# Kernel tuning notes

Hardware: AMD Instinct MI355X
Metric: run time of the kernel (lower is better)

## Reference

```python
import jax, jax.numpy as jnp
import numpy as np

INV_SQRT2 = 0.7071067811865476
BETA = 0.3
LN_EPS = 1e-5

B, S, P, C, TD = 128, 1024, 336, 128, 4
H1, H2, K = C // 4, C // 8, 3  # rda=4, rdb=8, ksize=3


def setup_inputs() -> dict:
    key = jax.random.key(0)
    ks = jax.random.split(key, 20)
    rn = lambda k, sh: jax.random.normal(k, sh, dtype=jnp.float32)
    return {
        "x": rn(ks[0], (B, S, C)),
        "x_mark_enc": rn(ks[1], (B, S, TD)),
        "x_dec": rn(ks[2], (B, P, C)),
        "y_mark_dec": rn(ks[3], (B, P, TD)),
        # time_enc params
        "W1": rn(ks[4], (H1, TD)) * 0.1, "b1": jnp.zeros((H1,), jnp.float32),
        "g1": jnp.ones((H1,), jnp.float32), "be1": jnp.zeros((H1,), jnp.float32),
        "W2": rn(ks[5], (H2, H1)) * 0.1, "b2": jnp.zeros((H2,), jnp.float32),
        "g2": jnp.ones((H2,), jnp.float32), "be2": jnp.zeros((H2,), jnp.float32),
        "Wc": rn(ks[6], (S, S, K)) * 0.02, "bc": jnp.zeros((S,), jnp.float32),
        "W3": rn(ks[7], (C, H2)) * 0.1, "b3": jnp.zeros((C,), jnp.float32),
        # projections
        "Wtp": rn(ks[8], (P, S)) * 0.02, "btp": jnp.zeros((P,), jnp.float32),
        "Whp": rn(ks[9], (P, S)) * 0.02, "bhp": jnp.zeros((P,), jnp.float32),
    }


def _haar_level1(x):
    # pywt.wavedec(sig, 'db1', level=1) -> [cA, cD]; concat along time.
    # For even length: cA[k]=(x[2k]+x[2k+1])/sqrt(2), cD[k]=(x[2k]-x[2k+1])/sqrt(2).
    xe, xo = x[:, 0::2, :], x[:, 1::2, :]
    cA = (xe + xo) * INV_SQRT2
    cD = (xe - xo) * INV_SQRT2
    return jnp.concatenate([cA, cD], axis=1)  # [B, S, C]


def _layernorm(h, g, b):
    m = jnp.mean(h, axis=-1, keepdims=True)
    v = jnp.mean((h - m) ** 2, axis=-1, keepdims=True)
    return (h - m) * jax.lax.rsqrt(v + LN_EPS) * g + b


def reference(x, x_mark_enc, x_dec, y_mark_dec,
              W1, b1, g1, be1, W2, b2, g2, be2, Wc, bc, W3, b3,
              Wtp, btp, Whp, bhp):
    # wavelet transform + instance norm over time (torch.var is unbiased)
    xw = _haar_level1(x)
    means = jnp.mean(xw, axis=1, keepdims=True)
    stdev = jnp.sqrt(jnp.var(xw, axis=1, ddof=1, keepdims=True) + 1e-5)
    xn = (xw - means) / stdev

    # time_enc MLP: Linear -> LN -> ReLU -> Linear -> LN -> ReLU
    h = jax.nn.relu(_layernorm(jnp.einsum('bst,ht->bsh', x_mark_enc, W1) + b1, g1, be1))
    h = jax.nn.relu(_layernorm(jnp.einsum('bsh,gh->bsg', h, W2) + b2, g2, be2))
    # Conv1d(in=seq_len, out=seq_len, k=3, padding='same') over feature dim H2
    h = jax.lax.conv_general_dilated(h, Wc, window_strides=(1,), padding='SAME',
                                     dimension_numbers=('NCH', 'OIH', 'NCH'))
    h = h + bc[None, :, None]
    time_embed = jnp.einsum('bsg,cg->bsc', h, W3) + b3  # [B, S, C]

    # seq->pred projections (Linear over time axis), then blend
    time_out = jnp.einsum('bsc,ps->bpc', time_embed, Wtp) + btp[None, :, None]
    pred = jnp.einsum('bsc,ps->bpc', xn, Whp) + bhp[None, :, None]
    pred = BETA * pred + (1.0 - BETA) * time_out
    pred = pred * stdev + means
    return pred  # [B, P, C] == dec_out[:, -pred_len:, :]
```

## Files before the change

kernel.cpp:

```cpp
#include <hip/hip_runtime.h>
#include <hip/hip_bf16.h>

#define INV_SQRT2f 0.70710678118654752440f
#define BETAf 0.3f
#define OMBf  0.7f
#define LN_EPSf 1e-5f

#define B 128
#define S 1024
#define P 336
#define C 128
#define H1 32
#define H2 16

#define WS_WHP2G  0
#define WS_EPI    262144
#define WS_BCP    296448
#define WS_H2     296832
#define WS_WCPT   2393984
#define WS_M      2393984
#define WS_AIMG   3426176

typedef short  s16x8 __attribute__((ext_vector_type(8)));
typedef float  f32x4 __attribute__((ext_vector_type(4)));

__device__ __forceinline__ unsigned f2bf(float f) {
    unsigned u = __float_as_uint(f);
    return (u + 0x7fffu + ((u >> 16) & 1u)) >> 16;
}

__device__ __forceinline__ int whp2l_u32(int p, int sp) {
    int kt   = sp >> 4;
    int tile = kt * 2 + p / 192;
    int sub  = (p % 192) >> 4;
    int kg   = (sp & 15) >> 2;
    int m    = p & 15;
    int byte = tile * 12288 + sub * 1024 + kg * 256 + m * 16 + 4 * (sp & 3);
    return byte >> 2;
}

__global__ void k_prep(const float* __restrict__ Whp, const float* __restrict__ Wtp,
                       const float* __restrict__ bc,  const float* __restrict__ bhp,
                       const float* __restrict__ btp, float* __restrict__ ws)
{
    const int p = blockIdx.x;
    const int t = threadIdx.x;
    unsigned* img = (unsigned*)ws;
    __shared__ float red[768];
    float sw = 0.f, rw = 0.f, bp = 0.f;
    for (int sp = t; sp < 512; sp += 256) {
        float a = Whp[p * 1024 + sp];
        float d = Whp[p * 1024 + 512 + sp];
        float va = BETAf * (a + d) * INV_SQRT2f;
        float vb = BETAf * (a - d) * INV_SQRT2f;
        img[whp2l_u32(p, sp)] = f2bf(va) | (f2bf(vb) << 16);
        sw += a + d;
    }
    for (int s = t; s < S; s += 256) {
        float w = Wtp[p * 1024 + s];
        rw += w;
        bp += w * bc[s];
    }
    red[t] = sw; red[256 + t] = rw; red[512 + t] = bp;
    __syncthreads();
    for (int off = 128; off > 0; off >>= 1) {
        if (t < off) {
            red[t]       += red[t + off];
            red[256 + t] += red[256 + t + off];
            red[512 + t] += red[512 + t + off];
        }
        __syncthreads();
    }
    if (t == 0) {
        ws[WS_BCP + p] = red[512];
        float* e = ws + WS_EPI + p * 4;
        e[0] = BETAf * bhp[p] + OMBf * btp[p];
        e[1] = OMBf * red[256];
        e[2] = 1.f - BETAf * red[0];
        e[3] = 0.f;
    }
}

__global__ void k_mlp(const float* __restrict__ xme,
                      const float* __restrict__ W1, const float* __restrict__ b1,
                      const float* __restrict__ g1, const float* __restrict__ be1,
                      const float* __restrict__ W2, const float* __restrict__ b2,
                      const float* __restrict__ g2, const float* __restrict__ be2,
                      float* __restrict__ ws)
{
    __shared__ float w1s[128], b1s[32], g1s[32], be1s[32];
    __shared__ float w2s[512], b2s[16], g2s[16], be2s[16];
    const int t = threadIdx.x;
    if (t < 128) w1s[t] = W1[t];
    if (t < 32) { b1s[t] = b1[t]; g1s[t] = g1[t]; be1s[t] = be1[t]; }
    for (int i = t; i < 512; i += 256) w2s[i] = W2[i];
    if (t < 16) { b2s[t] = b2[t]; g2s[t] = g2[t]; be2s[t] = be2[t]; }
    __syncthreads();

    const int row = blockIdx.x * 256 + t;
    float4 v = *(const float4*)(xme + (size_t)row * 4);

    float h1v[32];
    float m = 0.f;
    #pragma unroll
    for (int i = 0; i < 32; i++) {
        float a = w1s[i*4+0]*v.x + w1s[i*4+1]*v.y + w1s[i*4+2]*v.z + w1s[i*4+3]*v.w + b1s[i];
        h1v[i] = a; m += a;
    }
    m *= (1.f / 32.f);
    float var = 0.f;
    #pragma unroll
    for (int i = 0; i < 32; i++) { float d = h1v[i] - m; var += d * d; }
    var *= (1.f / 32.f);
    float rs = rsqrtf(var + LN_EPSf);
    #pragma unroll
    for (int i = 0; i < 32; i++)
        h1v[i] = fmaxf((h1v[i] - m) * rs * g1s[i] + be1s[i], 0.f);

    float h2v[16];
    float m2 = 0.f;
    #pragma unroll
    for (int g = 0; g < 16; g++) {
        float a = b2s[g];
        #pragma unroll
        for (int i = 0; i < 32; i++) a = fmaf(w2s[g * 32 + i], h1v[i], a);
        h2v[g] = a; m2 += a;
    }
    m2 *= (1.f / 16.f);
    float v2 = 0.f;
    #pragma unroll
    for (int g = 0; g < 16; g++) { float d = h2v[g] - m2; v2 += d * d; }
    v2 *= (1.f / 16.f);
    float rs2 = rsqrtf(v2 + LN_EPSf);
    float* h2o = ws + WS_H2 + (size_t)row * 16;
    #pragma unroll
    for (int g = 0; g < 16; g++)
        h2o[g] = fmaxf((h2v[g] - m2) * rs2 * g2s[g] + be2s[g], 0.f);
}

__global__ __launch_bounds__(256) void k_wcp(const float* __restrict__ Wc,
                                             const float* __restrict__ Wtp,
                                             float* __restrict__ ws)
{
    __shared__ __align__(16) unsigned short Bs[2][4][4][16][8];
    const int pbase = blockIdx.x * 96;
    const int n0    = blockIdx.y * 64;
    const int t     = threadIdx.x;
    const int lane  = t & 63;
    const int wid   = t >> 6;
    const int wm    = wid >> 1;
    const int wn    = wid & 1;
    const int g8    = lane >> 4;
    const int n16   = lane & 15;

    const int bn  = t & 63;
    const int bkg = t >> 6;

    int prow[3];
    #pragma unroll
    for (int fi = 0; fi < 3; fi++) {
        int pr = pbase + wm * 48 + fi * 16 + n16;
        prow[fi] = pr < P ? pr : P - 1;
    }

#define LOADB_(dst, kt) {                                                   \
    const float* xs_ = Wc + (size_t)((kt) * 32 + 8 * bkg) * 3072 + n0 + bn; \
    _Pragma("unroll")                                                       \
    for (int e_ = 0; e_ < 8; e_++) dst[e_] = xs_[(size_t)e_ * 3072]; }

#define WRITEB_(src, buf) {                                                 \
    uint4 w_;                                                               \
    w_.x = f2bf(src[0]) | (f2bf(src[1]) << 16);                             \
    w_.y = f2bf(src[2]) | (f2bf(src[3]) << 16);                             \
    w_.z = f2bf(src[4]) | (f2bf(src[5]) << 16);                             \
    w_.w = f2bf(src[6]) | (f2bf(src[7]) << 16);                             \
    *(uint4*)&Bs[buf][bn >> 4][bkg][bn & 15][0] = w_; }

#define LOADA_(dst, kt) {                                                   \
    _Pragma("unroll")                                                       \
    for (int fi_ = 0; fi_ < 3; fi_++) {                                     \
        const float* as_ = Wtp + (size_t)prow[fi_] * 1024 + (kt) * 32 + g8 * 8; \
        dst[fi_][0] = *(const float4*)(as_);                                \
        dst[fi_][1] = *(const float4*)(as_ + 4); } }

#define PACKA_(fa, src) {                                                   \
    _Pragma("unroll")                                                       \
    for (int fi_ = 0; fi_ < 3; fi_++) {                                     \
        uint4 w_;                                                           \
        w_.x = f2bf(src[fi_][0].x) | (f2bf(src[fi_][0].y) << 16);           \
        w_.y = f2bf(src[fi_][0].z) | (f2bf(src[fi_][0].w) << 16);           \
        w_.z = f2bf(src[fi_][1].x) | (f2bf(src[fi_][1].y) << 16);           \
        w_.w = f2bf(src[fi_][1].z) | (f2bf(src[fi_][1].w) << 16);           \
        fa[fi_] = *(s16x8*)&w_; } }

#define MFMA6_(buf, fa) {                                                   \
    s16x8 fb0 = *(const s16x8*)&Bs[buf][2 * wn + 0][g8][n16][0];            \
    s16x8 fb1 = *(const s16x8*)&Bs[buf][2 * wn + 1][g8][n16][0];            \
    _Pragma("unroll")                                                       \
    for (int fi_ = 0; fi_ < 3; fi_++) {                                     \
        acc[fi_][0] = __builtin_amdgcn_mfma_f32_16x16x32_bf16(fa[fi_], fb0, acc[fi_][0], 0, 0, 0); \
        acc[fi_][1] = __builtin_amdgcn_mfma_f32_16x16x32_bf16(fa[fi_], fb1, acc[fi_][1], 0, 0, 0); } }

    f32x4 acc[3][2];
    #pragma unroll
    for (int i = 0; i < 3; i++) {
        acc[i][0] = (f32x4){0.f, 0.f, 0.f, 0.f};
        acc[i][1] = (f32x4){0.f, 0.f, 0.f, 0.f};
    }

    float  b0r[8], b1r[8];
    float4 a0r[3][2], a1r[3][2];

    LOADA_(a0r, 0); LOADB_(b0r, 0);
    LOADA_(a1r, 1); LOADB_(b1r, 1);
    WRITEB_(b0r, 0);
    __syncthreads();

    for (int i = 0; i < 16; i++) {
        const int kt = 2 * i;
        {
            s16x8 fa[3];
            PACKA_(fa, a0r);
            if (kt + 2 < 32) { LOADA_(a0r, kt + 2); LOADB_(b0r, kt + 2); }
            MFMA6_(0, fa);
        }
        __syncthreads();
        WRITEB_(b1r, 1);
        __syncthreads();
        {
            s16x8 fa[3];
            PACKA_(fa, a1r);
            if (kt + 3 < 32) { LOADA_(a1r, kt + 3); LOADB_(b1r, kt + 3); }
            MFMA6_(1, fa);
        }
        __syncthreads();
        if (kt + 2 < 32) WRITEB_(b0r, 0);
        __syncthreads();
    }

#undef LOADB_
#undef WRITEB_
#undef LOADA_
#undef PACKA_
#undef MFMA6_

    float* wcT = ws + WS_WCPT;
    #pragma unroll
    for (int fi = 0; fi < 3; fi++) {
        #pragma unroll
        for (int r = 0; r < 4; r++) {
            int p = pbase + wm * 48 + fi * 16 + g8 * 4 + r;
            if (p < P) {
                wcT[(size_t)p * 3072 + n0 + wn * 32 + 0 * 16 + n16] = acc[fi][0][r];
                wcT[(size_t)p * 3072 + n0 + wn * 32 + 1 * 16 + n16] = acc[fi][1][r];
            }
        }
    }
}

__global__ void k_repack(float* __restrict__ ws)
{
    const int l  = threadIdx.x;
    const int ch = blockIdx.x;
    const int pf = blockIdx.y;
    const int k  = ch >> 5;
    const int i0 = (ch & 31) * 32 + (l >> 4) * 8;
    const int p  = pf * 16 + (l & 15);
    uint4 w = make_uint4(0, 0, 0, 0);
    if (p < P) {
        const float* wcT = ws + WS_WCPT + (size_t)p * 3072;
        float v[8];
        #pragma unroll
        for (int e = 0; e < 8; e++)
            v[e] = wcT[(i0 + e) * 3 + k];
        w.x = f2bf(v[0]) | (f2bf(v[1]) << 16);
        w.y = f2bf(v[2]) | (f2bf(v[3]) << 16);
        w.z = f2bf(v[4]) | (f2bf(v[5]) << 16);
        w.w = f2bf(v[6]) | (f2bf(v[7]) << 16);
    }
    ((uint4*)(ws + WS_AIMG))[(size_t)(ch * 24 + pf) * 64 + l] = w;
}

#define HT_RS 1056
__global__ __launch_bounds__(256) void k_mconv(float* __restrict__ ws)
{
    __shared__ unsigned short Ht[18 * HT_RS];
    const int b  = blockIdx.x;
    const int pt = blockIdx.y;
    const int t  = threadIdx.x;
    const int l  = t & 63;
    const int wid = t >> 6;
    const int pf = pt * 4 + wid;
    const int n16 = l & 15;
    const int g8  = l >> 4;

    for (int j = t; j < HT_RS; j += 256) {
        Ht[j] = 0;
        Ht[17 * HT_RS + j] = 0;
    }
    {
        const float* h2b = ws + WS_H2 + (size_t)b * 16384;
        const int s0 = t * 4;
        float v[4][16];
        #pragma unroll
        for (int rr = 0; rr < 4; rr++) {
            const float4* src = (const float4*)(h2b + (size_t)(s0 + rr) * 16);
            float4 a0 = src[0], a1 = src[1], a2 = src[2], a3 = src[3];
            v[rr][0]=a0.x; v[rr][1]=a0.y; v[rr][2]=a0.z; v[rr][3]=a0.w;
            v[rr][4]=a1.x; v[rr][5]=a1.y; v[rr][6]=a1.z; v[rr][7]=a1.w;
            v[rr][8]=a2.x; v[rr][9]=a2.y; v[rr][10]=a2.z; v[rr][11]=a2.w;
            v[rr][12]=a3.x; v[rr][13]=a3.y; v[rr][14]=a3.z; v[rr][15]=a3.w;
        }
        #pragma unroll
        for (int g = 0; g < 16; g++) {
            uint2 w;
            w.x = f2bf(v[0][g]) | (f2bf(v[1][g]) << 16);
            w.y = f2bf(v[2][g]) | (f2bf(v[3][g]) << 16);
            *(uint2*)&Ht[(g + 1) * HT_RS + s0] = w;
        }
    }
    __syncthreads();

    const uint4* ap = (const uint4*)(ws + WS_AIMG) + (size_t)pf * 64 + l;
    f32x4 acc = (f32x4){0.f, 0.f, 0.f, 0.f};
    uint4 fan = *ap;
    #pragma unroll 4
    for (int it = 0; it < 96; it++) {
        uint4 fac = fan;
        ap += 24 * 64;
        if (it < 95) fan = *ap;
        const int k  = it >> 5;
        const int kt = it & 31;
        s16x8 fb = *(const s16x8*)&Ht[(n16 + k) * HT_RS + kt * 32 + g8 * 8];
        s16x8 fa = *(s16x8*)&fac;
        acc = __builtin_amdgcn_mfma_f32_16x16x32_bf16(fa, fb, acc, 0, 0, 0);
    }

    #pragma unroll
    for (int r = 0; r < 4; r++) {
        int p = pf * 16 + g8 * 4 + r;
        if (p < P)
            ws[WS_M + ((size_t)b * P + p) * 16 + n16] = acc[r] + ws[WS_BCP + p];
    }
}

__global__ __launch_bounds__(256, 2) void k_pred(
    const float* __restrict__ x,
    const float* __restrict__ W3, const float* __restrict__ b3,
    const float* __restrict__ ws, float* __restrict__ out)
{
    __shared__ __align__(16) unsigned short Bs[2][8][4][16][8];
    __shared__ float sev[256], ssq[256], smean[128], sstd[128];
    const int b     = blockIdx.x;
    const int ptile = blockIdx.y;
    const int t     = threadIdx.x;
    const int lane  = t & 63;
    const int wid   = t >> 6;
    const int wm    = wid >> 1;
    const int wn    = wid & 1;
    const int g8    = lane >> 4;
    const int n16   = lane & 15;

    const float* xb = x + (size_t)b * S * C;
    const char* aimgc = (const char*)ws
        + ((ptile >> 1) * 12288)
        + (((ptile & 1) * 6 + wm * 3) * 1024)
        + (g8 * 256 + n16 * 16);

    f32x4 acc[3][4];
    #pragma unroll
    for (int i = 0; i < 3; i++)
        #pragma unroll
        for (int j = 0; j < 4; j++) acc[i][j] = (f32x4){0.f, 0.f, 0.f, 0.f};

    float ev_acc = 0.f, sq_acc = 0.f;

#define P_LOADB_(dst, kt) {                                                 \
    _Pragma("unroll")                                                       \
    for (int i_ = 0; i_ < 2; i_++) {                                        \
        int chunk_ = i_ * 256 + t;                                          \
        int c_ = chunk_ & 127, kg_ = chunk_ >> 7;                           \
        const float* xs_ = xb + (size_t)(32 * (kt) + 8 * kg_) * C + c_;     \
        _Pragma("unroll")                                                   \
        for (int e_ = 0; e_ < 8; e_++) dst[i_][e_] = xs_[(size_t)e_ * C]; } }

#define P_WRITEB_(src, buf) {                                               \
    _Pragma("unroll")                                                       \
    for (int i_ = 0; i_ < 2; i_++) {                                        \
        int chunk_ = i_ * 256 + t;                                          \
        int c_ = chunk_ & 127, kg_ = chunk_ >> 7;                           \
        uint4 w_;                                                           \
        w_.x = f2bf(src[i_][0]) | (f2bf(src[i_][1]) << 16);                 \
        w_.y = f2bf(src[i_][2]) | (f2bf(src[i_][3]) << 16);                 \
        w_.z = f2bf(src[i_][4]) | (f2bf(src[i_][5]) << 16);                 \
        w_.w = f2bf(src[i_][6]) | (f2bf(src[i_][7]) << 16);                 \
        *(uint4*)&Bs[buf][c_ >> 4][kg_][c_ & 15][0] = w_;                   \
        _Pragma("unroll")                                                   \
        for (int e_ = 0; e_ < 8; e_++) {                                    \
            float v_ = src[i_][e_];                                         \
            sq_acc = fmaf(v_, v_, sq_acc);                                  \
            if ((e_ & 1) == 0) ev_acc += v_;    \
        } } }

#define P_LOADA_(dst, kt) {                                                 \
    const char* ap_ = aimgc + (size_t)(kt) * 24576;                         \
    _Pragma("unroll")                                                       \
    for (int fi_ = 0; fi_ < 3; fi_++)                                       \
        dst[fi_] = *(const uint4*)(ap_ + fi_ * 1024); }

#define P_MFMA_(buf, au) {                                                  \
    s16x8 fb0 = *(const s16x8*)&Bs[buf][4 * wn + 0][g8][n16][0];            \
    s16x8 fb1 = *(const s16x8*)&Bs[buf][4 * wn + 1][g8][n16][0];            \
    s16x8 fb2 = *(const s16x8*)&Bs[buf][4 * wn + 2][g8][n16][0];            \
    s16x8 fb3 = *(const s16x8*)&Bs[buf][4 * wn + 3][g8][n16][0];            \
    _Pragma("unroll")                                                       \
    for (int fi_ = 0; fi_ < 3; fi_++) {                                     \
        s16x8 fa_ = *(s16x8*)&au[fi_];                                      \
        acc[fi_][0] = __builtin_amdgcn_mfma_f32_16x16x32_bf16(fa_, fb0, acc[fi_][0], 0, 0, 0); \
        acc[fi_][1] = __builtin_amdgcn_mfma_f32_16x16x32_bf16(fa_, fb1, acc[fi_][1], 0, 0, 0); \
        acc[fi_][2] = __builtin_amdgcn_mfma_f32_16x16x32_bf16(fa_, fb2, acc[fi_][2], 0, 0, 0); \
        acc[fi_][3] = __builtin_amdgcn_mfma_f32_16x16x32_bf16(fa_, fb3, acc[fi_][3], 0, 0, 0); } }

    float b0r[2][8], b1r[2][8];
    uint4 a0u[3], a1u[3];

    P_LOADA_(a0u, 0); P_LOADB_(b0r, 0);
    P_LOADA_(a1u, 1); P_LOADB_(b1r, 1);
    P_WRITEB_(b0r, 0);
    __syncthreads();

    for (int i = 0; i < 16; i++) {
        const int kt = 2 * i;
        {
            uint4 au[3];
            #pragma unroll
            for (int fi = 0; fi < 3; fi++) au[fi] = a0u[fi];
            if (kt + 2 < 32) { P_LOADA_(a0u, kt + 2); P_LOADB_(b0r, kt + 2); }
            P_MFMA_(0, au);
        }
        __syncthreads();
        P_WRITEB_(b1r, 1);
        __syncthreads();
        {
            uint4 au[3];
            #pragma unroll
            for (int fi = 0; fi < 3; fi++) au[fi] = a1u[fi];
            if (kt + 3 < 32) { P_LOADA_(a1u, kt + 3); P_LOADB_(b1r, kt + 3); }
            P_MFMA_(1, au);
        }
        __syncthreads();
        if (kt + 2 < 32) P_WRITEB_(b0r, 0);
        __syncthreads();
    }

#undef P_LOADB_
#undef P_WRITEB_
#undef P_LOADA_
#undef P_MFMA_

    sev[t] = ev_acc; ssq[t] = sq_acc;
    __syncthreads();
    if (t < 128) {
        float ev = sev[t] + sev[t + 128];
        float sq = ssq[t] + ssq[t + 128];
        float mean = ev * (INV_SQRT2f / 512.f);
        float var  = (sq - 1024.f * mean * mean) * (1.f / 1023.f);
        smean[t] = mean;
        sstd[t]  = sqrtf(var + LN_EPSf);
    }
    __syncthreads();

    const int cb = wn * 64 + n16;
    float sdv[4], mnv[4], b3v[4];
    f32x4 w3r[4][4];
    #pragma unroll
    for (int fj = 0; fj < 4; fj++) {
        int c = cb + fj * 16;
        sdv[fj] = sstd[c];
        mnv[fj] = smean[c];
        b3v[fj] = b3[c];
        const f32x4* wr = (const f32x4*)(W3 + c * 16);
        #pragma unroll
        for (int q = 0; q < 4; q++) w3r[fj][q] = wr[q];
    }
    const int prow0 = ptile * 96 + wm * 48 + g8 * 4;
    #pragma unroll
    for (int fi = 0; fi < 3; fi++) {
        #pragma unroll
        for (int r = 0; r < 4; r++) {
            int p  = prow0 + fi * 16 + r;
            int pc = p < P ? p : P - 1;
            const f32x4* mrow = (const f32x4*)(ws + WS_M + ((size_t)b * P + pc) * 16);
            f32x4 m0 = mrow[0], m1 = mrow[1], m2 = mrow[2], m3 = mrow[3];
            const float* e = ws + WS_EPI + pc * 4;
            float A13 = e[0], A4 = e[1], A2 = e[2];
            #pragma unroll
            for (int fj = 0; fj < 4; fj++) {
                float s = 0.f;
                #pragma unroll
                for (int q = 0; q < 4; q++) {
                    const f32x4 mv = (q==0)?m0:(q==1)?m1:(q==2)?m2:m3;
                    s = fmaf(mv.x, w3r[fj][q].x, s);
                    s = fmaf(mv.y, w3r[fj][q].y, s);
                    s = fmaf(mv.z, w3r[fj][q].z, s);
                    s = fmaf(mv.w, w3r[fj][q].w, s);
                }
                float res = acc[fi][fj][r]
                          + sdv[fj] * (OMBf * s + A13 + A4 * b3v[fj])
                          + A2 * mnv[fj];
                if (p < P)
                    out[((size_t)b * P + p) * C + cb + fj * 16] = res;
            }
        }
    }
}

extern "C" void kernel_launch(void* const* d_in, const int* in_sizes, int n_in,
                              void* d_out, int out_size, void* d_ws, size_t ws_size,
                              hipStream_t stream)
{
    const float* x    = (const float*)d_in[0];
    const float* xme  = (const float*)d_in[1];
    const float* W1   = (const float*)d_in[4];
    const float* b1   = (const float*)d_in[5];
    const float* g1   = (const float*)d_in[6];
    const float* be1  = (const float*)d_in[7];
    const float* W2   = (const float*)d_in[8];
    const float* b2   = (const float*)d_in[9];
    const float* g2   = (const float*)d_in[10];
    const float* be2  = (const float*)d_in[11];
    const float* Wc   = (const float*)d_in[12];
    const float* bc   = (const float*)d_in[13];
    const float* W3   = (const float*)d_in[14];
    const float* b3   = (const float*)d_in[15];
    const float* Wtp  = (const float*)d_in[16];
    const float* btp  = (const float*)d_in[17];
    const float* Whp  = (const float*)d_in[18];
    const float* bhp  = (const float*)d_in[19];
    float* ws  = (float*)d_ws;
    float* out = (float*)d_out;

    k_prep  <<<dim3(P),      dim3(256), 0, stream>>>(Whp, Wtp, bc, bhp, btp, ws);
    k_mlp   <<<dim3(512),    dim3(256), 0, stream>>>(xme, W1, b1, g1, be1,
                                                     W2, b2, g2, be2, ws);
    k_wcp   <<<dim3(4, 48),  dim3(256), 0, stream>>>(Wc, Wtp, ws);
    k_repack<<<dim3(96, 24), dim3(64),  0, stream>>>(ws);
    k_mconv <<<dim3(B, 6),   dim3(256), 0, stream>>>(ws);
    k_pred  <<<dim3(B, 4),   dim3(256), 0, stream>>>(x, W3, b3, ws, out);
}
```

Measured before the change: 109.6 us.

## Enlarge k_pred blocks to 512 threads covering 192 pred rows each

k_pred now runs 8 waves per block over 192 prediction rows instead of 4 waves over 96 rows, so each batch's x tile is staged into LDS and converted to bf16 half as many times. Every thread now loads a single 8-element chunk of x. The double-buffered loop is restructured to merge the LDS write of the next buffer into the compute phase, cutting the barriers per iteration from four to two. In exchange there are fewer blocks (256), and the larger blocks may reduce occupancy or add barrier wait time.

Result: faster. 104.7 us (-4.4%).

```diff
diff --git a/kernel.cpp b/kernel.cpp
--- a/kernel.cpp
+++ b/kernel.cpp
@@ -344,13 +344,13 @@
     }
 }
 
-__global__ __launch_bounds__(256, 2) void k_pred(
+__global__ __launch_bounds__(512, 1) void k_pred(
     const float* __restrict__ x,
     const float* __restrict__ W3, const float* __restrict__ b3,
     const float* __restrict__ ws, float* __restrict__ out)
 {
     __shared__ __align__(16) unsigned short Bs[2][8][4][16][8];
-    __shared__ float sev[256], ssq[256], smean[128], sstd[128];
+    __shared__ float sev[512], ssq[512], smean[128], sstd[128];
     const int b     = blockIdx.x;
     const int ptile = blockIdx.y;
     const int t     = threadIdx.x;
@@ -361,11 +361,12 @@
     const int g8    = lane >> 4;
     const int n16   = lane & 15;
 
+    const int sc  = t & 127;
+    const int skg = t >> 7;
+
     const float* xb = x + (size_t)b * S * C;
-    const char* aimgc = (const char*)ws
-        + ((ptile >> 1) * 12288)
-        + (((ptile & 1) * 6 + wm * 3) * 1024)
-        + (g8 * 256 + n16 * 16);
+    const char* aimgc = (const char*)ws + ptile * 12288
+        + (wm * 3) * 1024 + g8 * 256 + n16 * 16;
 
     f32x4 acc[3][4];
     #pragma unroll
@@ -376,31 +377,23 @@
     float ev_acc = 0.f, sq_acc = 0.f;
 
 #define P_LOADB_(dst, kt) {                                                 \
-    _Pragma("unroll")                                                       \
-    for (int i_ = 0; i_ < 2; i_++) {                                        \
-        int chunk_ = i_ * 256 + t;                                          \
-        int c_ = chunk_ & 127, kg_ = chunk_ >> 7;                           \
-        const float* xs_ = xb + (size_t)(32 * (kt) + 8 * kg_) * C + c_;     \
-        _Pragma("unroll")                                                   \
-        for (int e_ = 0; e_ < 8; e_++) dst[i_][e_] = xs_[(size_t)e_ * C]; } }
+    const float* xs_ = xb + (size_t)(32 * (kt) + 8 * skg) * C + sc;         \
+    _Pragma("unroll")                                                       \
+    for (int e_ = 0; e_ < 8; e_++) dst[e_] = xs_[(size_t)e_ * C]; }
 
 #define P_WRITEB_(src, buf) {                                               \
-    _Pragma("unroll")                                                       \
-    for (int i_ = 0; i_ < 2; i_++) {                                        \
-        int chunk_ = i_ * 256 + t;                                          \
-        int c_ = chunk_ & 127, kg_ = chunk_ >> 7;                           \
-        uint4 w_;                                                           \
-        w_.x = f2bf(src[i_][0]) | (f2bf(src[i_][1]) << 16);                 \
-        w_.y = f2bf(src[i_][2]) | (f2bf(src[i_][3]) << 16);                 \
-        w_.z = f2bf(src[i_][4]) | (f2bf(src[i_][5]) << 16);                 \
-        w_.w = f2bf(src[i_][6]) | (f2bf(src[i_][7]) << 16);                 \
-        *(uint4*)&Bs[buf][c_ >> 4][kg_][c_ & 15][0] = w_;                   \
-        _Pragma("unroll")                                                   \
-        for (int e_ = 0; e_ < 8; e_++) {                                    \
-            float v_ = src[i_][e_];                                         \
-            sq_acc = fmaf(v_, v_, sq_acc);                                  \
-            if ((e_ & 1) == 0) ev_acc += v_;    \
-        } } }
+    uint4 w_;                                                               \
+    w_.x = f2bf(src[0]) | (f2bf(src[1]) << 16);                             \
+    w_.y = f2bf(src[2]) | (f2bf(src[3]) << 16);                             \
+    w_.z = f2bf(src[4]) | (f2bf(src[5]) << 16);                             \
+    w_.w = f2bf(src[6]) | (f2bf(src[7]) << 16);                             \
+    *(uint4*)&Bs[buf][sc >> 4][skg][sc & 15][0] = w_;                       \
+    _Pragma("unroll")                                                       \
+    for (int e_ = 0; e_ < 8; e_++) {                                        \
+        float v_ = src[e_];                                                 \
+        sq_acc = fmaf(v_, v_, sq_acc);                                      \
+        if ((e_ & 1) == 0) ev_acc += v_;    \
+    } }
 
 #define P_LOADA_(dst, kt) {                                                 \
     const char* ap_ = aimgc + (size_t)(kt) * 24576;                         \
@@ -421,11 +414,11 @@
         acc[fi_][2] = __builtin_amdgcn_mfma_f32_16x16x32_bf16(fa_, fb2, acc[fi_][2], 0, 0, 0); \
         acc[fi_][3] = __builtin_amdgcn_mfma_f32_16x16x32_bf16(fa_, fb3, acc[fi_][3], 0, 0, 0); } }
 
-    float b0r[2][8], b1r[2][8];
+    float b0r[8], b1r[8];
     uint4 a0u[3], a1u[3];
 
-    P_LOADA_(a0u, 0); P_LOADB_(b0r, 0);
-    P_LOADA_(a1u, 1); P_LOADB_(b1r, 1);
+    P_LOADB_(b0r, 0); P_LOADB_(b1r, 1);
+    P_LOADA_(a0u, 0); P_LOADA_(a1u, 1);
     P_WRITEB_(b0r, 0);
     __syncthreads();
 
@@ -437,20 +430,19 @@
             for (int fi = 0; fi < 3; fi++) au[fi] = a0u[fi];
             if (kt + 2 < 32) { P_LOADA_(a0u, kt + 2); P_LOADB_(b0r, kt + 2); }
             P_MFMA_(0, au);
-        }
-        __syncthreads();
-        P_WRITEB_(b1r, 1);
-        __syncthreads();
+            P_WRITEB_(b1r, 1);
+            __syncthreads();
+        }
         {
+            const int kt1 = kt + 1;
             uint4 au[3];
             #pragma unroll
             for (int fi = 0; fi < 3; fi++) au[fi] = a1u[fi];
-            if (kt + 3 < 32) { P_LOADA_(a1u, kt + 3); P_LOADB_(b1r, kt + 3); }
+            if (kt1 + 2 < 32) { P_LOADA_(a1u, kt1 + 2); P_LOADB_(b1r, kt1 + 2); }
             P_MFMA_(1, au);
-        }
-        __syncthreads();
-        if (kt + 2 < 32) P_WRITEB_(b0r, 0);
-        __syncthreads();
+            if (kt1 < 31) P_WRITEB_(b0r, 0);
+            __syncthreads();
+        }
     }
 
 #undef P_LOADB_
@@ -461,8 +453,8 @@
     sev[t] = ev_acc; ssq[t] = sq_acc;
     __syncthreads();
     if (t < 128) {
-        float ev = sev[t] + sev[t + 128];
-        float sq = ssq[t] + ssq[t + 128];
+        float ev = sev[t] + sev[t + 128] + sev[t + 256] + sev[t + 384];
+        float sq = ssq[t] + ssq[t + 128] + ssq[t + 256] + ssq[t + 384];
         float mean = ev * (INV_SQRT2f / 512.f);
         float var  = (sq - 1024.f * mean * mean) * (1.f / 1023.f);
         smean[t] = mean;
@@ -483,7 +475,7 @@
         #pragma unroll
         for (int q = 0; q < 4; q++) w3r[fj][q] = wr[q];
     }
-    const int prow0 = ptile * 96 + wm * 48 + g8 * 4;
+    const int prow0 = ptile * 192 + wm * 48 + g8 * 4;
     #pragma unroll
     for (int fi = 0; fi < 3; fi++) {
         #pragma unroll
@@ -546,5 +538,5 @@
     k_wcp   <<<dim3(4, 48),  dim3(256), 0, stream>>>(Wc, Wtp, ws);
     k_repack<<<dim3(96, 24), dim3(64),  0, stream>>>(ws);
     k_mconv <<<dim3(B, 6),   dim3(256), 0, stream>>>(ws);
-    k_pred  <<<dim3(B, 4),   dim3(256), 0, stream>>>(x, W3, b3, ws, out);
-}
+    k_pred  <<<dim3(B, 2),   dim3(512), 0, stream>>>(x, W3, b3, ws, out);
+}
```
